# Optimization experiments

Hardware: AMD Instinct MI355X
Metric: run time of the kernel (lower is better)

The kernel has to match this reference:

```python
import jax, jax.numpy as jnp
import numpy as np

NEG_INF = -9e15
ALPHA = 0.2  # LeakyReLU negative slope used by GraphAttentionLayer


def gat_layer(h, adj, W, a, concat):
    # h: [N, din], W: [din, dout], a: [2*dout, 1]
    Wh = h @ W                              # [N, dout]
    dout = W.shape[1]
    f1 = Wh @ a[:dout]                      # [N, 1]
    f2 = Wh @ a[dout:]                      # [N, 1]
    e = jax.nn.leaky_relu(f1 + f2.T, negative_slope=ALPHA)   # [N, N]
    att = jax.nn.softmax(jnp.where(adj > 0, e, NEG_INF), axis=1)
    hp = att @ Wh                           # [N, dout]
    out = jax.nn.elu(hp) if concat else hp
    return out, att


def setup_inputs() -> dict:
    key = jax.random.key(0)
    ks = jax.random.split(key, 6)
    N, d_in, d_hid, d_out = 8192, 256, 128, 64
    features = jax.random.normal(ks[0], (N, d_in), dtype=jnp.float32)
    adj = (jax.random.uniform(ks[1], (N, N)) < 0.01).astype(jnp.float32)
    s = 0.1
    W1 = jax.random.normal(ks[2], (d_in, d_hid), dtype=jnp.float32) * s
    a1 = jax.random.normal(ks[3], (2 * d_hid, 1), dtype=jnp.float32) * s
    W2 = jax.random.normal(ks[4], (d_hid, d_out), dtype=jnp.float32) * s
    a2 = jax.random.normal(ks[5], (2 * d_out, 1), dtype=jnp.float32) * s
    return {"features": features, "adj": adj, "W1": W1, "a1": a1, "W2": W2, "a2": a2}


def reference(features, adj, W1, a1, W2, a2):
    h1, attention = gat_layer(features, adj, W1, a1, concat=True)   # gat1 (elu)
    h2, _ = gat_layer(h1, adj, W2, a2, concat=False)                 # gat2
    row_mask = (adj.sum(axis=1) > 0).astype(h2.dtype)[:, None]       # [N, 1]
    genenet_res = jax.nn.sigmoid(h2 @ h2.T) * row_mask               # inner-product decoder
    return h2, genenet_res, attention
```

## Files before the change

kernel.cpp:

```cpp
#include <hip/hip_runtime.h>
#include <cstdint>
#include <cstddef>

#define NN 8192
#define DIN 256
#define DHID 128
#define DOUT 64
#define MAXDEG 256

using short8  = __attribute__((ext_vector_type(8))) short;
using floatx4 = __attribute__((ext_vector_type(4))) float;

__device__ inline unsigned short f2bf(float x) {
  union { float f; unsigned u; } c; c.f = x;
  unsigned r = (c.u + 0x7FFFu + ((c.u >> 16) & 1u)) >> 16;
  return (unsigned short)r;
}

__global__ __launch_bounds__(256) void k_gemm1(const float* __restrict__ feat,
                                               const float* __restrict__ W1,
                                               float* __restrict__ Wh1) {
  __shared__ float Ws[64 * DHID];
  __shared__ float Fs[64][65];
  const int tid = threadIdx.x;
  const int cx = tid & 31;
  const int ry = tid >> 5;
  const int r0 = blockIdx.x * 64;
  float acc[8][4] = {};
  for (int kc = 0; kc < DIN; kc += 64) {
    const float4* src = (const float4*)(W1 + (size_t)kc * DHID);
    float4* dst = (float4*)Ws;
    #pragma unroll
    for (int i = 0; i < 8; ++i) dst[i * 256 + tid] = src[i * 256 + tid];
    #pragma unroll
    for (int i = 0; i < 4; ++i) {
      int idx = i * 256 + tid;
      int row = idx >> 4, kq = idx & 15;
      float4 v = *(const float4*)(feat + (size_t)(r0 + row) * DIN + kc + kq * 4);
      Fs[row][kq * 4 + 0] = v.x; Fs[row][kq * 4 + 1] = v.y;
      Fs[row][kq * 4 + 2] = v.z; Fs[row][kq * 4 + 3] = v.w;
    }
    __syncthreads();
    #pragma unroll 4
    for (int k = 0; k < 64; ++k) {
      float4 w = *(const float4*)(Ws + k * DHID + cx * 4);
      #pragma unroll
      for (int r = 0; r < 8; ++r) {
        float f = Fs[ry * 8 + r][k];
        acc[r][0] += f * w.x; acc[r][1] += f * w.y;
        acc[r][2] += f * w.z; acc[r][3] += f * w.w;
      }
    }
    __syncthreads();
  }
  #pragma unroll
  for (int r = 0; r < 8; ++r) {
    float4 o = make_float4(acc[r][0], acc[r][1], acc[r][2], acc[r][3]);
    *(float4*)(Wh1 + (size_t)(r0 + ry * 8 + r) * DHID + cx * 4) = o;
  }
}

__global__ __launch_bounds__(256) void k_gemm2(const float* __restrict__ h1,
                                               const float* __restrict__ W2,
                                               float* __restrict__ Wh2) {
  __shared__ float Ws[64 * DOUT];
  __shared__ float Fs[128][65];
  const int tid = threadIdx.x;
  const int cx = tid & 15;
  const int ry = tid >> 4;
  const int r0 = blockIdx.x * 128;
  float acc[8][4] = {};
  for (int kc = 0; kc < DHID; kc += 64) {
    const float4* src = (const float4*)(W2 + (size_t)kc * DOUT);
    float4* dst = (float4*)Ws;
    #pragma unroll
    for (int i = 0; i < 4; ++i) dst[i * 256 + tid] = src[i * 256 + tid];
    #pragma unroll
    for (int i = 0; i < 8; ++i) {
      int idx = i * 256 + tid;
      int row = idx >> 4, kq = idx & 15;
      float4 v = *(const float4*)(h1 + (size_t)(r0 + row) * DHID + kc + kq * 4);
      Fs[row][kq * 4 + 0] = v.x; Fs[row][kq * 4 + 1] = v.y;
      Fs[row][kq * 4 + 2] = v.z; Fs[row][kq * 4 + 3] = v.w;
    }
    __syncthreads();
    #pragma unroll 4
    for (int k = 0; k < 64; ++k) {
      float4 w = *(const float4*)(Ws + k * DOUT + cx * 4);
      #pragma unroll
      for (int r = 0; r < 8; ++r) {
        float f = Fs[ry * 8 + r][k];
        acc[r][0] += f * w.x; acc[r][1] += f * w.y;
        acc[r][2] += f * w.z; acc[r][3] += f * w.w;
      }
    }
    __syncthreads();
  }
  #pragma unroll
  for (int r = 0; r < 8; ++r) {
    float4 o = make_float4(acc[r][0], acc[r][1], acc[r][2], acc[r][3]);
    *(float4*)(Wh2 + (size_t)(r0 + ry * 8 + r) * DOUT + cx * 4) = o;
  }
}

__global__ __launch_bounds__(256) void k_fvec1(const float* __restrict__ Wh1,
                                               const float* __restrict__ a1,
                                               float* __restrict__ f1, float* __restrict__ f2) {
  int wv = threadIdx.x >> 6, lane = threadIdx.x & 63;
  int row = blockIdx.x * 4 + wv;
  float2 x = *(const float2*)(Wh1 + (size_t)row * DHID + lane * 2);
  float2 u = *(const float2*)(a1 + lane * 2);
  float2 v = *(const float2*)(a1 + DHID + lane * 2);
  float s1 = x.x * u.x + x.y * u.y;
  float s2 = x.x * v.x + x.y * v.y;
  #pragma unroll
  for (int off = 32; off; off >>= 1) { s1 += __shfl_down(s1, off); s2 += __shfl_down(s2, off); }
  if (lane == 0) { f1[row] = s1; f2[row] = s2; }
}

__global__ __launch_bounds__(256) void k_fvec2(const float* __restrict__ Wh2,
                                               const float* __restrict__ a2,
                                               float* __restrict__ f1, float* __restrict__ f2) {
  int wv = threadIdx.x >> 6, lane = threadIdx.x & 63;
  int row = blockIdx.x * 4 + wv;
  float x = Wh2[(size_t)row * DOUT + lane];
  float s1 = x * a2[lane];
  float s2 = x * a2[DOUT + lane];
  #pragma unroll
  for (int off = 32; off; off >>= 1) { s1 += __shfl_down(s1, off); s2 += __shfl_down(s2, off); }
  if (lane == 0) { f1[row] = s1; f2[row] = s2; }
}

__global__ __launch_bounds__(256) void k_att1(const float* __restrict__ adj,
                                              const float* __restrict__ f1v,
                                              const float* __restrict__ f2v,
                                              const float* __restrict__ Wh1,
                                              float* __restrict__ att_out,
                                              float* __restrict__ h1,
                                              int* __restrict__ csr,
                                              int* __restrict__ degree) {
  __shared__ int    scols[MAXDEG];
  __shared__ float  sval[MAXDEG];
  __shared__ float  xred[8];
  __shared__ float2 red2[256];
  __shared__ int    cnt;
  const int tid = threadIdx.x;
  const int row = blockIdx.x;
  const int wv = tid >> 6, lane = tid & 63;
  if (tid == 0) cnt = 0;
  __syncthreads();
  const float4* arow = (const float4*)(adj + (size_t)row * NN);
  float4 v[8];
  #pragma unroll
  for (int it = 0; it < 8; ++it) v[it] = arow[it * 256 + tid];
  #pragma unroll
  for (int it = 0; it < 8; ++it) {
    int base4 = (it * 256 + tid) * 4;
    if (v[it].x > 0.0f) { int s = atomicAdd(&cnt, 1); if (s < MAXDEG) scols[s] = base4; }
    if (v[it].y > 0.0f) { int s = atomicAdd(&cnt, 1); if (s < MAXDEG) scols[s] = base4 + 1; }
    if (v[it].z > 0.0f) { int s = atomicAdd(&cnt, 1); if (s < MAXDEG) scols[s] = base4 + 2; }
    if (v[it].w > 0.0f) { int s = atomicAdd(&cnt, 1); if (s < MAXDEG) scols[s] = base4 + 3; }
  }
  __syncthreads();
  const int deg = min(cnt, MAXDEG);
  if (tid == 0) degree[row] = deg;
  int col = -1; float e = -3.0e38f;
  if (tid < deg) {
    col = scols[tid];
    csr[(size_t)row * MAXDEG + tid] = col;
    float t = f1v[row] + f2v[col];
    e = t > 0.0f ? t : 0.2f * t;
  }
  float m = e;
  #pragma unroll
  for (int off = 32; off; off >>= 1) m = fmaxf(m, __shfl_xor(m, off));
  if (lane == 0) xred[wv] = m;
  __syncthreads();
  m = fmaxf(fmaxf(xred[0], xred[1]), fmaxf(xred[2], xred[3]));
  float ex = (tid < deg) ? __expf(e - m) : 0.0f;
  float sm = ex;
  #pragma unroll
  for (int off = 32; off; off >>= 1) sm += __shfl_xor(sm, off);
  if (lane == 0) xred[4 + wv] = sm;
  __syncthreads();
  const float inv = 1.0f / (xred[4] + xred[5] + xred[6] + xred[7]);
  const float p = ex * inv;
  if (tid < deg) sval[tid] = p;
  const float fill = (deg == 0) ? (1.0f / (float)NN) : 0.0f;
  float4 fv = make_float4(fill, fill, fill, fill);
  float4* orow = (float4*)(att_out + (size_t)row * NN);
  #pragma unroll
  for (int it = 0; it < 8; ++it) orow[it * 256 + tid] = fv;
  __syncthreads();
  if (tid < deg) att_out[(size_t)row * NN + col] = p;
  const int g = tid >> 6;
  float2 acc = make_float2(0.0f, 0.0f);
  if (deg > 0) {
    for (int t = g; t < deg; t += 4) {
      float sv = sval[t];
      float2 w = *(const float2*)(Wh1 + (size_t)scols[t] * DHID + lane * 2);
      acc.x += sv * w.x; acc.y += sv * w.y;
    }
  } else {
    for (int r = g; r < NN; r += 4) {
      float2 w = *(const float2*)(Wh1 + (size_t)r * DHID + lane * 2);
      acc.x += w.x; acc.y += w.y;
    }
    acc.x *= (1.0f / (float)NN); acc.y *= (1.0f / (float)NN);
  }
  red2[tid] = acc;
  __syncthreads();
  if (tid < 64) {
    float2 a0 = red2[tid], a1 = red2[tid + 64], a2 = red2[tid + 128], a3 = red2[tid + 192];
    float hx = a0.x + a1.x + a2.x + a3.x;
    float hy = a0.y + a1.y + a2.y + a3.y;
    hx = hx > 0.0f ? hx : (__expf(hx) - 1.0f);
    hy = hy > 0.0f ? hy : (__expf(hy) - 1.0f);
    *(float2*)(h1 + (size_t)row * DHID + tid * 2) = make_float2(hx, hy);
  }
}

__global__ __launch_bounds__(256) void k_att2(const int* __restrict__ csr,
                                              const int* __restrict__ degree,
                                              const float* __restrict__ f1v,
                                              const float* __restrict__ f2v,
                                              const float* __restrict__ Wh2,
                                              float* __restrict__ h2) {
  __shared__ int   scols[MAXDEG];
  __shared__ float sval[MAXDEG];
  __shared__ float xred[8];
  __shared__ float red[256];
  const int tid = threadIdx.x;
  const int row = blockIdx.x;
  const int wv = tid >> 6, lane = tid & 63;
  const int deg = degree[row];
  int col = -1; float e = -3.0e38f;
  if (tid < deg) {
    col = csr[(size_t)row * MAXDEG + tid];
    scols[tid] = col;
    float t = f1v[row] + f2v[col];
    e = t > 0.0f ? t : 0.2f * t;
  }
  float m = e;
  #pragma unroll
  for (int off = 32; off; off >>= 1) m = fmaxf(m, __shfl_xor(m, off));
  if (lane == 0) xred[wv] = m;
  __syncthreads();
  m = fmaxf(fmaxf(xred[0], xred[1]), fmaxf(xred[2], xred[3]));
  float ex = (tid < deg) ? __expf(e - m) : 0.0f;
  float sm = ex;
  #pragma unroll
  for (int off = 32; off; off >>= 1) sm += __shfl_xor(sm, off);
  if (lane == 0) xred[4 + wv] = sm;
  __syncthreads();
  const float inv = 1.0f / (xred[4] + xred[5] + xred[6] + xred[7]);
  if (tid < deg) sval[tid] = ex * inv;
  __syncthreads();
  const int g = tid >> 6;
  float acc = 0.0f;
  if (deg > 0) {
    for (int t = g; t < deg; t += 4) acc += sval[t] * Wh2[(size_t)scols[t] * DOUT + lane];
  } else {
    for (int r = g; r < NN; r += 4) acc += Wh2[(size_t)r * DOUT + lane];
    acc *= (1.0f / (float)NN);
  }
  red[tid] = acc;
  __syncthreads();
  if (tid < 64) h2[(size_t)row * DOUT + tid] = red[tid] + red[tid + 64] + red[tid + 128] + red[tid + 192];
}

__global__ __launch_bounds__(256) void k_genenet(const float* __restrict__ h2,
                                                 const int* __restrict__ degree,
                                                 float* __restrict__ out) {
  __shared__ unsigned short As[128 * 64];
  __shared__ unsigned short Bs[128 * 64];
  __shared__ float dmask[128];
  const int tid = threadIdx.x;
  const int R0 = blockIdx.x * 128, C0 = blockIdx.y * 128;
  #pragma unroll
  for (int it = 0; it < 8; ++it) {
    int idx = it * 256 + tid;
    int r = idx >> 4, kq = idx & 15;
    int c = kq >> 1, hf = kq & 1;
    int off = r * 64 + (((c + r) & 7) << 3) + (hf << 2);
    float4 va = *(const float4*)(h2 + (size_t)(R0 + r) * DOUT + kq * 4);
    float4 vb = *(const float4*)(h2 + (size_t)(C0 + r) * DOUT + kq * 4);
    ushort4 ba = make_ushort4(f2bf(va.x), f2bf(va.y), f2bf(va.z), f2bf(va.w));
    ushort4 bb = make_ushort4(f2bf(vb.x), f2bf(vb.y), f2bf(vb.z), f2bf(vb.w));
    *(ushort4*)&As[off] = ba;
    *(ushort4*)&Bs[off] = bb;
  }
  if (tid < 128) dmask[tid] = (degree[R0 + tid] > 0) ? 1.0f : 0.0f;
  __syncthreads();
  const int wave = tid >> 6, lane = tid & 63;
  const int wr = wave >> 1, wc = wave & 1;
  const int lr = lane & 15, quad = lane >> 4;
  short8 a[4][2], b[4][2];
  #pragma unroll
  for (int mi = 0; mi < 4; ++mi) {
    int r = wr * 64 + mi * 16 + lr;
    #pragma unroll
    for (int j = 0; j < 2; ++j) {
      int c = quad + 4 * j;
      a[mi][j] = *(const short8*)(const void*)&As[r * 64 + (((c + r) & 7) << 3)];
    }
  }
  #pragma unroll
  for (int ni = 0; ni < 4; ++ni) {
    int r = wc * 64 + ni * 16 + lr;
    #pragma unroll
    for (int j = 0; j < 2; ++j) {
      int c = quad + 4 * j;
      b[ni][j] = *(const short8*)(const void*)&Bs[r * 64 + (((c + r) & 7) << 3)];
    }
  }
  floatx4 acc[4][4] = {};
  #pragma unroll
  for (int mi = 0; mi < 4; ++mi)
    #pragma unroll
    for (int ni = 0; ni < 4; ++ni) {
      acc[mi][ni] = __builtin_amdgcn_mfma_f32_16x16x32_bf16(a[mi][0], b[ni][0], acc[mi][ni], 0, 0, 0);
      acc[mi][ni] = __builtin_amdgcn_mfma_f32_16x16x32_bf16(a[mi][1], b[ni][1], acc[mi][ni], 0, 0, 0);
    }
  #pragma unroll
  for (int mi = 0; mi < 4; ++mi) {
    #pragma unroll
    for (int reg = 0; reg < 4; ++reg) {
      int lrow = wr * 64 + mi * 16 + quad * 4 + reg;
      float msk = dmask[lrow];
      size_t rowoff = (size_t)(R0 + lrow) * NN + C0 + wc * 64;
      #pragma unroll
      for (int ni = 0; ni < 4; ++ni) {
        float x = acc[mi][ni][reg];
        float s = __builtin_amdgcn_rcpf(1.0f + __expf(-x));
        out[rowoff + ni * 16 + lr] = s * msk;
      }
    }
  }
}

extern "C" void kernel_launch(void* const* d_in, const int* in_sizes, int n_in,
                              void* d_out, int out_size, void* d_ws, size_t ws_size,
                              hipStream_t stream) {
  const float* feat = (const float*)d_in[0];
  const float* adj  = (const float*)d_in[1];
  const float* W1   = (const float*)d_in[2];
  const float* a1   = (const float*)d_in[3];
  const float* W2   = (const float*)d_in[4];
  const float* a2   = (const float*)d_in[5];
  float* out = (float*)d_out;
  float* h2_out  = out;
  float* gen_out = out + (size_t)NN * DOUT;
  float* att_out = gen_out + (size_t)NN * NN;
  int*   csr  = (int*)gen_out;
  float* Wh1  = gen_out + 2097152;
  float* h1   = gen_out + 3145728;
  float* Wh2  = gen_out + 4194304;
  float* f1_1 = gen_out + 4718592;
  float* f2_1 = f1_1 + NN;
  float* f1_2 = f2_1 + NN;
  float* f2_2 = f1_2 + NN;
  int* degree = (int*)d_ws;

  k_gemm1  <<<dim3(NN / 64),  dim3(256), 0, stream>>>(feat, W1, Wh1);
  k_fvec1  <<<dim3(NN / 4),   dim3(256), 0, stream>>>(Wh1, a1, f1_1, f2_1);
  k_att1   <<<dim3(NN),       dim3(256), 0, stream>>>(adj, f1_1, f2_1, Wh1, att_out, h1, csr, degree);
  k_gemm2  <<<dim3(NN / 128), dim3(256), 0, stream>>>(h1, W2, Wh2);
  k_fvec2  <<<dim3(NN / 4),   dim3(256), 0, stream>>>(Wh2, a2, f1_2, f2_2);
  k_att2   <<<dim3(NN),       dim3(256), 0, stream>>>(csr, degree, f1_2, f2_2, Wh2, h2_out);
  k_genenet<<<dim3(64, 64),   dim3(256), 0, stream>>>(h2_out, degree, gen_out);
}
```

Before: 803.1 us.

## Use one wave per row in attention kernels, stage genenet stores, shrink GEMM tiles

The attention kernels now map one wavefront to each row, four rows per block. This removes cross-wave LDS reductions and block barriers from the softmax and aggregation, while each wave scans its own whole adjacency row. The GEMM kernels use smaller row tiles so more blocks launch. The genenet epilogue stages MFMA results through shared memory so the sigmoid output is written with coalesced float4 stores. The trade-off is less parallelism per row in the gather loop and extra LDS traffic and barriers in the epilogue.

```diff
diff --git a/kernel.cpp b/kernel.cpp
--- a/kernel.cpp
+++ b/kernel.cpp
@@ -21,19 +21,19 @@
                                                const float* __restrict__ W1,
                                                float* __restrict__ Wh1) {
   __shared__ float Ws[64 * DHID];
-  __shared__ float Fs[64][65];
+  __shared__ float Fs[32][65];
   const int tid = threadIdx.x;
   const int cx = tid & 31;
   const int ry = tid >> 5;
-  const int r0 = blockIdx.x * 64;
-  float acc[8][4] = {};
+  const int r0 = blockIdx.x * 32;
+  float acc[4][4] = {};
   for (int kc = 0; kc < DIN; kc += 64) {
     const float4* src = (const float4*)(W1 + (size_t)kc * DHID);
     float4* dst = (float4*)Ws;
     #pragma unroll
     for (int i = 0; i < 8; ++i) dst[i * 256 + tid] = src[i * 256 + tid];
     #pragma unroll
-    for (int i = 0; i < 4; ++i) {
+    for (int i = 0; i < 2; ++i) {
       int idx = i * 256 + tid;
       int row = idx >> 4, kq = idx & 15;
       float4 v = *(const float4*)(feat + (size_t)(r0 + row) * DIN + kc + kq * 4);
@@ -45,8 +45,8 @@
     for (int k = 0; k < 64; ++k) {
       float4 w = *(const float4*)(Ws + k * DHID + cx * 4);
       #pragma unroll
-      for (int r = 0; r < 8; ++r) {
-        float f = Fs[ry * 8 + r][k];
+      for (int r = 0; r < 4; ++r) {
+        float f = Fs[ry * 4 + r][k];
         acc[r][0] += f * w.x; acc[r][1] += f * w.y;
         acc[r][2] += f * w.z; acc[r][3] += f * w.w;
       }
@@ -54,9 +54,9 @@
     __syncthreads();
   }
   #pragma unroll
-  for (int r = 0; r < 8; ++r) {
+  for (int r = 0; r < 4; ++r) {
     float4 o = make_float4(acc[r][0], acc[r][1], acc[r][2], acc[r][3]);
-    *(float4*)(Wh1 + (size_t)(r0 + ry * 8 + r) * DHID + cx * 4) = o;
+    *(float4*)(Wh1 + (size_t)(r0 + ry * 4 + r) * DHID + cx * 4) = o;
   }
 }
 
@@ -64,19 +64,19 @@
                                                const float* __restrict__ W2,
                                                float* __restrict__ Wh2) {
   __shared__ float Ws[64 * DOUT];
-  __shared__ float Fs[128][65];
+  __shared__ float Fs[32][65];
   const int tid = threadIdx.x;
   const int cx = tid & 15;
   const int ry = tid >> 4;
-  const int r0 = blockIdx.x * 128;
-  float acc[8][4] = {};
+  const int r0 = blockIdx.x * 32;
+  float acc[2][4] = {};
   for (int kc = 0; kc < DHID; kc += 64) {
     const float4* src = (const float4*)(W2 + (size_t)kc * DOUT);
     float4* dst = (float4*)Ws;
     #pragma unroll
     for (int i = 0; i < 4; ++i) dst[i * 256 + tid] = src[i * 256 + tid];
     #pragma unroll
-    for (int i = 0; i < 8; ++i) {
+    for (int i = 0; i < 2; ++i) {
       int idx = i * 256 + tid;
       int row = idx >> 4, kq = idx & 15;
       float4 v = *(const float4*)(h1 + (size_t)(r0 + row) * DHID + kc + kq * 4);
@@ -88,8 +88,8 @@
     for (int k = 0; k < 64; ++k) {
       float4 w = *(const float4*)(Ws + k * DOUT + cx * 4);
       #pragma unroll
-      for (int r = 0; r < 8; ++r) {
-        float f = Fs[ry * 8 + r][k];
+      for (int r = 0; r < 2; ++r) {
+        float f = Fs[ry * 2 + r][k];
         acc[r][0] += f * w.x; acc[r][1] += f * w.y;
         acc[r][2] += f * w.z; acc[r][3] += f * w.w;
       }
@@ -97,9 +97,9 @@
     __syncthreads();
   }
   #pragma unroll
-  for (int r = 0; r < 8; ++r) {
+  for (int r = 0; r < 2; ++r) {
     float4 o = make_float4(acc[r][0], acc[r][1], acc[r][2], acc[r][3]);
-    *(float4*)(Wh2 + (size_t)(r0 + ry * 8 + r) * DOUT + cx * 4) = o;
+    *(float4*)(Wh2 + (size_t)(r0 + ry * 2 + r) * DOUT + cx * 4) = o;
   }
 }
 
@@ -139,85 +139,86 @@
                                               float* __restrict__ h1,
                                               int* __restrict__ csr,
                                               int* __restrict__ degree) {
-  __shared__ int    scols[MAXDEG];
-  __shared__ float  sval[MAXDEG];
-  __shared__ float  xred[8];
-  __shared__ float2 red2[256];
-  __shared__ int    cnt;
-  const int tid = threadIdx.x;
-  const int row = blockIdx.x;
-  const int wv = tid >> 6, lane = tid & 63;
-  if (tid == 0) cnt = 0;
+  __shared__ int   scols[4][MAXDEG];
+  __shared__ float sval[4][MAXDEG];
+  __shared__ int   cnt[4];
+  const int tid = threadIdx.x;
+  const int wid = tid >> 6, lane = tid & 63;
+  const int row = blockIdx.x * 4 + wid;
+  if (lane == 0) cnt[wid] = 0;
   __syncthreads();
   const float4* arow = (const float4*)(adj + (size_t)row * NN);
-  float4 v[8];
-  #pragma unroll
-  for (int it = 0; it < 8; ++it) v[it] = arow[it * 256 + tid];
-  #pragma unroll
-  for (int it = 0; it < 8; ++it) {
-    int base4 = (it * 256 + tid) * 4;
-    if (v[it].x > 0.0f) { int s = atomicAdd(&cnt, 1); if (s < MAXDEG) scols[s] = base4; }
-    if (v[it].y > 0.0f) { int s = atomicAdd(&cnt, 1); if (s < MAXDEG) scols[s] = base4 + 1; }
-    if (v[it].z > 0.0f) { int s = atomicAdd(&cnt, 1); if (s < MAXDEG) scols[s] = base4 + 2; }
-    if (v[it].w > 0.0f) { int s = atomicAdd(&cnt, 1); if (s < MAXDEG) scols[s] = base4 + 3; }
-  }
-  __syncthreads();
-  const int deg = min(cnt, MAXDEG);
-  if (tid == 0) degree[row] = deg;
-  int col = -1; float e = -3.0e38f;
-  if (tid < deg) {
-    col = scols[tid];
-    csr[(size_t)row * MAXDEG + tid] = col;
-    float t = f1v[row] + f2v[col];
-    e = t > 0.0f ? t : 0.2f * t;
-  }
-  float m = e;
+  #pragma unroll 4
+  for (int it = 0; it < 32; ++it) {
+    float4 v = arow[it * 64 + lane];
+    int base = (it * 64 + lane) * 4;
+    if (v.x > 0.0f) { int s = atomicAdd(&cnt[wid], 1); if (s < MAXDEG) scols[wid][s] = base; }
+    if (v.y > 0.0f) { int s = atomicAdd(&cnt[wid], 1); if (s < MAXDEG) scols[wid][s] = base + 1; }
+    if (v.z > 0.0f) { int s = atomicAdd(&cnt[wid], 1); if (s < MAXDEG) scols[wid][s] = base + 2; }
+    if (v.w > 0.0f) { int s = atomicAdd(&cnt[wid], 1); if (s < MAXDEG) scols[wid][s] = base + 3; }
+  }
+  __syncthreads();
+  const int deg = min(cnt[wid], MAXDEG);
+  if (lane == 0) degree[row] = deg;
+  const float fillv = (deg == 0) ? (1.0f / (float)NN) : 0.0f;
+  float4 fv = make_float4(fillv, fillv, fillv, fillv);
+  float4* orow = (float4*)(att_out + (size_t)row * NN);
+  #pragma unroll 8
+  for (int it = 0; it < 32; ++it) orow[it * 64 + lane] = fv;
+  for (int t = lane; t < deg; t += 64) csr[(size_t)row * MAXDEG + t] = scols[wid][t];
+  const float f1r = f1v[row];
+  float e[4]; int cols[4];
+  float m = -3.0e38f;
+  #pragma unroll
+  for (int j = 0; j < 4; ++j) {
+    int t = lane + j * 64;
+    cols[j] = 0; e[j] = -3.0e38f;
+    if (t < deg) {
+      int c = scols[wid][t]; cols[j] = c;
+      float x = f1r + f2v[c];
+      e[j] = x > 0.0f ? x : 0.2f * x;
+    }
+    m = fmaxf(m, e[j]);
+  }
   #pragma unroll
   for (int off = 32; off; off >>= 1) m = fmaxf(m, __shfl_xor(m, off));
-  if (lane == 0) xred[wv] = m;
-  __syncthreads();
-  m = fmaxf(fmaxf(xred[0], xred[1]), fmaxf(xred[2], xred[3]));
-  float ex = (tid < deg) ? __expf(e - m) : 0.0f;
-  float sm = ex;
-  #pragma unroll
-  for (int off = 32; off; off >>= 1) sm += __shfl_xor(sm, off);
-  if (lane == 0) xred[4 + wv] = sm;
-  __syncthreads();
-  const float inv = 1.0f / (xred[4] + xred[5] + xred[6] + xred[7]);
-  const float p = ex * inv;
-  if (tid < deg) sval[tid] = p;
-  const float fill = (deg == 0) ? (1.0f / (float)NN) : 0.0f;
-  float4 fv = make_float4(fill, fill, fill, fill);
-  float4* orow = (float4*)(att_out + (size_t)row * NN);
-  #pragma unroll
-  for (int it = 0; it < 8; ++it) orow[it * 256 + tid] = fv;
-  __syncthreads();
-  if (tid < deg) att_out[(size_t)row * NN + col] = p;
-  const int g = tid >> 6;
+  float ex[4]; float s = 0.0f;
+  #pragma unroll
+  for (int j = 0; j < 4; ++j) {
+    ex[j] = __expf(e[j] - m);
+    if (lane + j * 64 >= deg) ex[j] = 0.0f;
+    s += ex[j];
+  }
+  #pragma unroll
+  for (int off = 32; off; off >>= 1) s += __shfl_xor(s, off);
+  const float inv = 1.0f / s;
+  #pragma unroll
+  for (int j = 0; j < 4; ++j) { int t = lane + j * 64; if (t < deg) sval[wid][t] = ex[j] * inv; }
+  asm volatile("s_waitcnt vmcnt(0)" ::: "memory");
+  #pragma unroll
+  for (int j = 0; j < 4; ++j) {
+    int t = lane + j * 64;
+    if (t < deg) att_out[(size_t)row * NN + cols[j]] = ex[j] * inv;
+  }
+  __syncthreads();
   float2 acc = make_float2(0.0f, 0.0f);
   if (deg > 0) {
-    for (int t = g; t < deg; t += 4) {
-      float sv = sval[t];
-      float2 w = *(const float2*)(Wh1 + (size_t)scols[t] * DHID + lane * 2);
+    #pragma unroll 4
+    for (int t = 0; t < deg; ++t) {
+      float sv = sval[wid][t];
+      float2 w = *(const float2*)(Wh1 + (size_t)scols[wid][t] * DHID + lane * 2);
       acc.x += sv * w.x; acc.y += sv * w.y;
     }
   } else {
-    for (int r = g; r < NN; r += 4) {
+    for (int r = 0; r < NN; ++r) {
       float2 w = *(const float2*)(Wh1 + (size_t)r * DHID + lane * 2);
       acc.x += w.x; acc.y += w.y;
     }
     acc.x *= (1.0f / (float)NN); acc.y *= (1.0f / (float)NN);
   }
-  red2[tid] = acc;
-  __syncthreads();
-  if (tid < 64) {
-    float2 a0 = red2[tid], a1 = red2[tid + 64], a2 = red2[tid + 128], a3 = red2[tid + 192];
-    float hx = a0.x + a1.x + a2.x + a3.x;
-    float hy = a0.y + a1.y + a2.y + a3.y;
-    hx = hx > 0.0f ? hx : (__expf(hx) - 1.0f);
-    hy = hy > 0.0f ? hy : (__expf(hy) - 1.0f);
-    *(float2*)(h1 + (size_t)row * DHID + tid * 2) = make_float2(hx, hy);
-  }
+  float hx = acc.x > 0.0f ? acc.x : (__expf(acc.x) - 1.0f);
+  float hy = acc.y > 0.0f ? acc.y : (__expf(acc.y) - 1.0f);
+  *(float2*)(h1 + (size_t)row * DHID + lane * 2) = make_float2(hx, hy);
 }
 
 __global__ __launch_bounds__(256) void k_att2(const int* __restrict__ csr,
@@ -226,55 +227,61 @@
                                               const float* __restrict__ f2v,
                                               const float* __restrict__ Wh2,
                                               float* __restrict__ h2) {
-  __shared__ int   scols[MAXDEG];
-  __shared__ float sval[MAXDEG];
-  __shared__ float xred[8];
-  __shared__ float red[256];
-  const int tid = threadIdx.x;
-  const int row = blockIdx.x;
-  const int wv = tid >> 6, lane = tid & 63;
+  __shared__ int   scols[4][MAXDEG];
+  __shared__ float sval[4][MAXDEG];
+  const int tid = threadIdx.x;
+  const int wid = tid >> 6, lane = tid & 63;
+  const int row = blockIdx.x * 4 + wid;
   const int deg = degree[row];
-  int col = -1; float e = -3.0e38f;
-  if (tid < deg) {
-    col = csr[(size_t)row * MAXDEG + tid];
-    scols[tid] = col;
-    float t = f1v[row] + f2v[col];
-    e = t > 0.0f ? t : 0.2f * t;
-  }
-  float m = e;
+  const float f1r = f1v[row];
+  float e[4]; int cols[4];
+  float m = -3.0e38f;
+  #pragma unroll
+  for (int j = 0; j < 4; ++j) {
+    int t = lane + j * 64;
+    cols[j] = 0; e[j] = -3.0e38f;
+    if (t < deg) {
+      int c = csr[(size_t)row * MAXDEG + t];
+      cols[j] = c; scols[wid][t] = c;
+      float x = f1r + f2v[c];
+      e[j] = x > 0.0f ? x : 0.2f * x;
+    }
+    m = fmaxf(m, e[j]);
+  }
   #pragma unroll
   for (int off = 32; off; off >>= 1) m = fmaxf(m, __shfl_xor(m, off));
-  if (lane == 0) xred[wv] = m;
-  __syncthreads();
-  m = fmaxf(fmaxf(xred[0], xred[1]), fmaxf(xred[2], xred[3]));
-  float ex = (tid < deg) ? __expf(e - m) : 0.0f;
-  float sm = ex;
-  #pragma unroll
-  for (int off = 32; off; off >>= 1) sm += __shfl_xor(sm, off);
-  if (lane == 0) xred[4 + wv] = sm;
-  __syncthreads();
-  const float inv = 1.0f / (xred[4] + xred[5] + xred[6] + xred[7]);
-  if (tid < deg) sval[tid] = ex * inv;
-  __syncthreads();
-  const int g = tid >> 6;
+  float ex[4]; float s = 0.0f;
+  #pragma unroll
+  for (int j = 0; j < 4; ++j) {
+    ex[j] = __expf(e[j] - m);
+    if (lane + j * 64 >= deg) ex[j] = 0.0f;
+    s += ex[j];
+  }
+  #pragma unroll
+  for (int off = 32; off; off >>= 1) s += __shfl_xor(s, off);
+  const float inv = 1.0f / s;
+  #pragma unroll
+  for (int j = 0; j < 4; ++j) { int t = lane + j * 64; if (t < deg) sval[wid][t] = ex[j] * inv; }
+  __syncthreads();
   float acc = 0.0f;
   if (deg > 0) {
-    for (int t = g; t < deg; t += 4) acc += sval[t] * Wh2[(size_t)scols[t] * DOUT + lane];
+    #pragma unroll 4
+    for (int t = 0; t < deg; ++t)
+      acc += sval[wid][t] * Wh2[(size_t)scols[wid][t] * DOUT + lane];
   } else {
-    for (int r = g; r < NN; r += 4) acc += Wh2[(size_t)r * DOUT + lane];
+    for (int r = 0; r < NN; ++r) acc += Wh2[(size_t)r * DOUT + lane];
     acc *= (1.0f / (float)NN);
   }
-  red[tid] = acc;
-  __syncthreads();
-  if (tid < 64) h2[(size_t)row * DOUT + tid] = red[tid] + red[tid + 64] + red[tid + 128] + red[tid + 192];
+  h2[(size_t)row * DOUT + lane] = acc;
 }
 
 __global__ __launch_bounds__(256) void k_genenet(const float* __restrict__ h2,
                                                  const int* __restrict__ degree,
                                                  float* __restrict__ out) {
-  __shared__ unsigned short As[128 * 64];
-  __shared__ unsigned short Bs[128 * 64];
+  __shared__ __align__(16) unsigned short AB[2 * 128 * 64];
   __shared__ float dmask[128];
+  unsigned short* As = AB;
+  unsigned short* Bs = AB + 128 * 64;
   const int tid = threadIdx.x;
   const int R0 = blockIdx.x * 128, C0 = blockIdx.y * 128;
   #pragma unroll
@@ -322,20 +329,36 @@
       acc[mi][ni] = __builtin_amdgcn_mfma_f32_16x16x32_bf16(a[mi][0], b[ni][0], acc[mi][ni], 0, 0, 0);
       acc[mi][ni] = __builtin_amdgcn_mfma_f32_16x16x32_bf16(a[mi][1], b[ni][1], acc[mi][ni], 0, 0, 0);
     }
-  #pragma unroll
-  for (int mi = 0; mi < 4; ++mi) {
-    #pragma unroll
-    for (int reg = 0; reg < 4; ++reg) {
-      int lrow = wr * 64 + mi * 16 + quad * 4 + reg;
-      float msk = dmask[lrow];
-      size_t rowoff = (size_t)(R0 + lrow) * NN + C0 + wc * 64;
+  __syncthreads();
+  float* stage = (float*)AB;
+  #pragma unroll
+  for (int half = 0; half < 2; ++half) {
+    if (wr == half) {
       #pragma unroll
-      for (int ni = 0; ni < 4; ++ni) {
-        float x = acc[mi][ni][reg];
-        float s = __builtin_amdgcn_rcpf(1.0f + __expf(-x));
-        out[rowoff + ni * 16 + lr] = s * msk;
-      }
-    }
+      for (int mi = 0; mi < 4; ++mi)
+        #pragma unroll
+        for (int reg = 0; reg < 4; ++reg) {
+          int lrow = mi * 16 + quad * 4 + reg;
+          #pragma unroll
+          for (int ni = 0; ni < 4; ++ni)
+            stage[lrow * 128 + wc * 64 + ni * 16 + lr] = acc[mi][ni][reg];
+        }
+    }
+    __syncthreads();
+    #pragma unroll
+    for (int it = 0; it < 8; ++it) {
+      int idx = it * 256 + tid;
+      int r = idx >> 5, c4 = idx & 31;
+      float4 x = *(const float4*)&stage[r * 128 + c4 * 4];
+      float msk = dmask[half * 64 + r];
+      float4 o;
+      o.x = msk * __builtin_amdgcn_rcpf(1.0f + __expf(-x.x));
+      o.y = msk * __builtin_amdgcn_rcpf(1.0f + __expf(-x.y));
+      o.z = msk * __builtin_amdgcn_rcpf(1.0f + __expf(-x.z));
+      o.w = msk * __builtin_amdgcn_rcpf(1.0f + __expf(-x.w));
+      *(float4*)(out + (size_t)(R0 + half * 64 + r) * NN + C0 + c4 * 4) = o;
+    }
+    if (half == 0) __syncthreads();
   }
 }
 
@@ -362,11 +385,11 @@
   float* f2_2 = f1_2 + NN;
   int* degree = (int*)d_ws;
 
-  k_gemm1  <<<dim3(NN / 64),  dim3(256), 0, stream>>>(feat, W1, Wh1);
-  k_fvec1  <<<dim3(NN / 4),   dim3(256), 0, stream>>>(Wh1, a1, f1_1, f2_1);
-  k_att1   <<<dim3(NN),       dim3(256), 0, stream>>>(adj, f1_1, f2_1, Wh1, att_out, h1, csr, degree);
-  k_gemm2  <<<dim3(NN / 128), dim3(256), 0, stream>>>(h1, W2, Wh2);
-  k_fvec2  <<<dim3(NN / 4),   dim3(256), 0, stream>>>(Wh2, a2, f1_2, f2_2);
-  k_att2   <<<dim3(NN),       dim3(256), 0, stream>>>(csr, degree, f1_2, f2_2, Wh2, h2_out);
-  k_genenet<<<dim3(64, 64),   dim3(256), 0, stream>>>(h2_out, degree, gen_out);
-}
+  k_gemm1  <<<dim3(NN / 32), dim3(256), 0, stream>>>(feat, W1, Wh1);
+  k_fvec1  <<<dim3(NN / 4),  dim3(256), 0, stream>>>(Wh1, a1, f1_1, f2_1);
+  k_att1   <<<dim3(NN / 4),  dim3(256), 0, stream>>>(adj, f1_1, f2_1, Wh1, att_out, h1, csr, degree);
+  k_gemm2  <<<dim3(NN / 32), dim3(256), 0, stream>>>(h1, W2, Wh2);
+  k_fvec2  <<<dim3(NN / 4),  dim3(256), 0, stream>>>(Wh2, a2, f1_2, f2_2);
+  k_att2   <<<dim3(NN / 4),  dim3(256), 0, stream>>>(csr, degree, f1_2, f2_2, Wh2, h2_out);
+  k_genenet<<<dim3(64, 64),  dim3(256), 0, stream>>>(h2_out, degree, gen_out);
+}
```

Result: no change. 812.8 us (+1.2%).
